# Kernel optimization log

Hardware: AMD Instinct MI355X
Metric: run time of the kernel (lower is better)

Reference implementation:

```python
import jax, jax.numpy as jnp
from jax import lax
import numpy as np

DIM = 768        # d_model (mamba-130m)
D_IN = 1024      # vision encoder feature dim
NQ = 384         # num_queries
NB = 12          # num_blocks
BATCH = 2
LSEQ = 1024      # image tokens
DI = 2 * DIM     # mamba d_inner (expand=2)
DS = 16          # d_state
DC = 4           # d_conv
DTR = 48         # dt_rank = ceil(768/16)
NH = 16          # attention heads
HD = DIM // NH
NM = NB + 2      # mamba instances: fwd-enc, bwd-enc, one per block


def _ln(x, g, b):
    m = jnp.mean(x, -1, keepdims=True)
    v = jnp.mean((x - m) ** 2, -1, keepdims=True)
    return (x - m) * lax.rsqrt(v + 1e-5) * g + b


def _mamba(x, in_w, conv_w, conv_b, xproj_w, dt_w, dt_b, A_log, Dp, out_w):
    # x: (B, L, DIM)
    Bb = x.shape[0]
    xz = x @ in_w.T                      # (B, L, 2*DI)
    xi, z = jnp.split(xz, 2, -1)
    # depthwise causal conv1d over time
    xc = lax.conv_general_dilated(xi.transpose(0, 2, 1), conv_w[:, None, :], (1,),
                                  [(DC - 1, 0)], feature_group_count=DI,
                                  dimension_numbers=('NCH', 'OIH', 'NCH'))
    xc = jax.nn.silu((xc + conv_b[None, :, None]).transpose(0, 2, 1))  # (B, L, DI)
    dbl = xc @ xproj_w.T                 # (B, L, DTR + 2*DS)
    dt, Bm, Cm = jnp.split(dbl, [DTR, DTR + DS], -1)
    dt = jax.nn.softplus(dt @ dt_w.T + dt_b)   # (B, L, DI)
    A = -jnp.exp(A_log)                        # (DI, DS)
    dA = jnp.exp(dt[..., None] * A)            # (B, L, DI, DS)
    dBx = dt[..., None] * Bm[:, :, None, :] * xc[..., None]

    def step(h, inp):
        dA_t, dBx_t, C_t = inp
        h = dA_t * h + dBx_t
        return h, jnp.einsum('bds,bs->bd', h, C_t)

    h0 = jnp.zeros((Bb, DI, DS), x.dtype)
    _, ys = lax.scan(step, h0, (dA.transpose(1, 0, 2, 3), dBx.transpose(1, 0, 2, 3), Cm.transpose(1, 0, 2)))
    y = ys.transpose(1, 0, 2) + Dp * xc
    y = y * jax.nn.silu(z)
    return y @ out_w.T


def _local_allowed(nq, nk):
    # matches Attention.get_local_mask: query i attends to its contiguous key block
    kpq, extra = nk // nq, nk % nq
    i = jnp.arange(nq)
    start = i * kpq + jnp.minimum(i, extra)
    end = start + kpq + (i < extra)
    k = jnp.arange(nk)
    return (k[None, :] >= start[:, None]) & (k[None, :] < end[:, None])


def _mha(q_in, kv, in_w, in_b, out_w, out_b, allowed):
    # nn.MultiheadAttention(dim, 16, batch_first=True) cross-attention
    wq, wk, wv = jnp.split(in_w, 3, 0)
    bq, bk, bv = jnp.split(in_b, 3, 0)
    Bb = q_in.shape[0]
    q = (q_in @ wq.T + bq).reshape(Bb, -1, NH, HD)
    k = (kv @ wk.T + bk).reshape(Bb, -1, NH, HD)
    v = (kv @ wv.T + bv).reshape(Bb, -1, NH, HD)
    s = jnp.einsum('bqhd,bkhd->bhqk', q, k) / np.float32(np.sqrt(HD))
    s = jnp.where(allowed[None, None], s, -jnp.inf)
    a = jax.nn.softmax(s, -1)
    o = jnp.einsum('bhqk,bkhd->bqhd', a, v).reshape(Bb, -1, DIM)
    return o @ out_w.T + out_b


def _model(img_emb, queries, vision_proj_w, vision_proj_b, ln_vision_g, ln_vision_b,
           mamba_in_w, mamba_conv_w, mamba_conv_b, mamba_xproj_w, mamba_dt_w, mamba_dt_b,
           mamba_A_log, mamba_D, mamba_out_w, seq_norm_g, seq_norm_b,
           attn_in_w, attn_in_b, attn_out_w, attn_out_b, cross_w, cross_b):
    mp = lambda i: (mamba_in_w[i], mamba_conv_w[i], mamba_conv_b[i], mamba_xproj_w[i],
                    mamba_dt_w[i], mamba_dt_b[i], mamba_A_log[i], mamba_D[i], mamba_out_w[i])
    feats = _ln(img_emb @ vision_proj_w.T + vision_proj_b, ln_vision_g, ln_vision_b)
    fwd = _mamba(feats, *mp(0))
    bwd = jnp.flip(_mamba(jnp.flip(feats, 1), *mp(1)), 1)
    c = fwd + bwd + feats
    x = jnp.broadcast_to(queries, (img_emb.shape[0], NQ, DIM))
    allowed = _local_allowed(NQ, c.shape[1])
    for l in range(NB):
        x = _ln(x, seq_norm_g[l], seq_norm_b[l])
        x = _mamba(x, *mp(l + 2)) + x
        score = _mha(x, c, attn_in_w[l], attn_in_b[l], attn_out_w[l], attn_out_b[l], allowed)
        x = jnp.concatenate([x, score], -1) @ cross_w[l].T + cross_b[l]
    return x


_model_jit = jax.jit(_model)


def setup_inputs() -> dict:
    key = jax.random.key(0)
    ks = iter(jax.random.split(key, 24))
    rn = lambda shape, s=0.02: jax.random.normal(next(ks), shape, jnp.float32) * s
    A_log = jnp.broadcast_to(jnp.log(jnp.arange(1, DS + 1, dtype=jnp.float32)), (NM, DI, DS))
    return {
        'img_emb': rn((BATCH, LSEQ, D_IN), 1.0),
        'queries': rn((1, NQ, DIM)),
        'vision_proj_w': rn((DIM, D_IN)),
        'vision_proj_b': jnp.zeros((DIM,), jnp.float32),
        'ln_vision_g': jnp.ones((DIM,), jnp.float32),
        'ln_vision_b': jnp.zeros((DIM,), jnp.float32),
        'mamba_in_w': rn((NM, 2 * DI, DIM)),
        'mamba_conv_w': rn((NM, DI, DC), 0.1),
        'mamba_conv_b': jnp.zeros((NM, DI), jnp.float32),
        'mamba_xproj_w': rn((NM, DTR + 2 * DS, DI)),
        'mamba_dt_w': rn((NM, DI, DTR), 0.1),
        'mamba_dt_b': rn((NM, DI), 0.5),
        'mamba_A_log': A_log,
        'mamba_D': jnp.ones((NM, DI), jnp.float32),
        'mamba_out_w': rn((NM, DIM, DI)),
        'seq_norm_g': jnp.ones((NB, DIM), jnp.float32),
        'seq_norm_b': jnp.zeros((NB, DIM), jnp.float32),
        'attn_in_w': rn((NB, 3 * DIM, DIM)),
        'attn_in_b': jnp.zeros((NB, 3 * DIM), jnp.float32),
        'attn_out_w': rn((NB, DIM, DIM)),
        'attn_out_b': jnp.zeros((NB, DIM), jnp.float32),
        'cross_w': rn((NB, DIM, 2 * DIM)),
        'cross_b': jnp.zeros((NB, DIM), jnp.float32),
    }


def reference(img_emb, queries, vision_proj_w, vision_proj_b, ln_vision_g, ln_vision_b,
              mamba_in_w, mamba_conv_w, mamba_conv_b, mamba_xproj_w, mamba_dt_w, mamba_dt_b,
              mamba_A_log, mamba_D, mamba_out_w, seq_norm_g, seq_norm_b,
              attn_in_w, attn_in_b, attn_out_w, attn_out_b, cross_w, cross_b):
    return _model_jit(img_emb, queries, vision_proj_w, vision_proj_b, ln_vision_g, ln_vision_b,
                      mamba_in_w, mamba_conv_w, mamba_conv_b, mamba_xproj_w, mamba_dt_w, mamba_dt_b,
                      mamba_A_log, mamba_D, mamba_out_w, seq_norm_g, seq_norm_b,
                      attn_in_w, attn_in_b, attn_out_w, attn_out_b, cross_w, cross_b)
```

## Files before the change

### kernel.cpp

```cpp
#include <hip/hip_runtime.h>
#include <hip/hip_bf16.h>

#define DIMQ 768
#define D_IN 1024
#define NQ 384
#define NBK 12
#define BATCH 2
#define LSEQ 1024
#define DI 1536
#define DS 16
#define DTR 48
#define NH 16
#define HD 48

typedef __attribute__((ext_vector_type(8))) short short8;
typedef __attribute__((ext_vector_type(4))) float f32x4;

#define GF_BIAS 1
#define GF_SOFTPLUS 2
#define EPI_BIAS 1
#define EPI_ADDT 2

#define LOG2E 1.4426950408889634f

__device__ __forceinline__ unsigned short f2bf(float f) {
    unsigned int u = __builtin_bit_cast(unsigned int, f);
    u = (u + 0x7FFFu + ((u >> 16) & 1u)) >> 16;
    return (unsigned short)u;
}
__device__ __forceinline__ float bf2f(unsigned short h) {
    unsigned int u = ((unsigned int)h) << 16;
    return __builtin_bit_cast(float, u);
}

__device__ __forceinline__ void gload_lds16(const void* g, void* l) {
    __builtin_amdgcn_global_load_lds(
        (const __attribute__((address_space(1))) void*)g,
        (__attribute__((address_space(3))) void*)l, 16, 0, 0);
}

struct WTab {
    const float* src[10];
    long long dstOff[10];
    long long ps[10];
    int cum[10];
    int rows[10], cols[10], dcols[10];
    int n;
    int total;
};

__global__ void wconv_kernel(unsigned short* __restrict__ dst, WTab T)
{
    const int i = blockIdx.x * 256 + threadIdx.x;
    if (i >= T.total) return;
    int sI = 0;
    while (i >= T.cum[sI]) ++sI;
    const int e = i - (sI ? T.cum[sI - 1] : 0);
    const int dcols = T.dcols[sI];
    const int r = e / dcols;
    const int c = e - r * dcols;
    float v = 0.f;
    if (r < T.rows[sI] && c < T.cols[sI]) v = T.src[sI][(long long)r * T.cols[sI] + c];
    const unsigned short h = f2bf(v);
    const unsigned short l = f2bf(v - bf2f(h));
    dst[T.dstOff[sI] + e] = h;
    dst[T.dstOff[sI] + T.ps[sI] + e] = l;
}

__global__ __launch_bounds__(256, 3)
void gemm_direct(const float* __restrict__ Ag, const unsigned short* __restrict__ Bhl,
                 float* __restrict__ Cg, const float* __restrict__ biasg,
                 int M, int N, int K, int lda, int ldb, int ldc,
                 long long sA, long long sB, long long sC, long long sBias,
                 long long planeB, int flags)
{
    __shared__ __align__(16) unsigned short As[2][2][64][40];
    __shared__ __align__(16) unsigned short Bs[2][2][128][32];

    const int z = blockIdx.z;
    const float* A = Ag + (size_t)z * sA;
    const unsigned short* Bhi = Bhl + (size_t)z * sB;
    const unsigned short* Blo = Bhi + planeB;
    float* C = Cg + (size_t)z * sC;

    const int mBase = blockIdx.x * 64;
    const int nBase = blockIdx.y * 128;
    const int tid = threadIdx.x, lane = tid & 63, wave = tid >> 6;
    const int lm = lane & 15, lq = lane >> 4;
    const int wn = wave * 32;
    const int arow = tid >> 2, aq = tid & 3;
    const int brow = lane >> 2;
    const int bcol = (lane & 3) * 8;

    const int ktiles = (K + 31) >> 5;

    auto issueB = [&](int t, int buf) {
#pragma unroll
        for (int cc = 0; cc < 4; ++cc) {
            const int chunk = wave * 4 + cc;
            const int pl = chunk >> 3;
            const int r16 = chunk & 7;
            const unsigned short* bp = pl ? Blo : Bhi;
            const int n = nBase + r16 * 16 + brow;
            gload_lds16(bp + (size_t)n * ldb + t * 32 + bcol, &Bs[buf][pl][r16 * 16][0]);
        }
    };
    auto loadA = [&](int t, float* v) {
        const int col = t * 32 + aq * 8;
        const float* src = A + (size_t)(mBase + arow) * lda + col;
#pragma unroll
        for (int u = 0; u < 2; ++u) {
            float4 t4 = make_float4(0.f, 0.f, 0.f, 0.f);
            if (col + u * 4 < K) t4 = *(const float4*)(src + u * 4);
            v[u*4+0]=t4.x; v[u*4+1]=t4.y; v[u*4+2]=t4.z; v[u*4+3]=t4.w;
        }
    };
    auto writeA = [&](const float* v, int buf) {
        short8 ph, plv;
#pragma unroll
        for (int j = 0; j < 8; ++j) {
            unsigned short h = f2bf(v[j]);
            ph[j] = (short)h;
            plv[j] = (short)f2bf(v[j] - bf2f(h));
        }
        *(short8*)&As[buf][0][arow][aq * 8] = ph;
        *(short8*)&As[buf][1][arow][aq * 8] = plv;
    };

    float av[8];
    issueB(0, 0);
    loadA(0, av);
    writeA(av, 0);

    f32x4 acc[4][2] = {};
    for (int t = 0; t < ktiles; ++t) {
        const int buf = t & 1;
        __syncthreads();
        const bool more = (t + 1) < ktiles;
        if (more) { issueB(t + 1, buf ^ 1); loadA(t + 1, av); }
        short8 ah[4], al[4], bh[2], bl[2];
#pragma unroll
        for (int i = 0; i < 4; ++i) {
            ah[i] = *(const short8*)&As[buf][0][16*i + lm][lq * 8];
            al[i] = *(const short8*)&As[buf][1][16*i + lm][lq * 8];
        }
#pragma unroll
        for (int j = 0; j < 2; ++j) {
            bh[j] = *(const short8*)&Bs[buf][0][wn + 16*j + lm][lq * 8];
            bl[j] = *(const short8*)&Bs[buf][1][wn + 16*j + lm][lq * 8];
        }
#pragma unroll
        for (int i = 0; i < 4; ++i)
#pragma unroll
            for (int j = 0; j < 2; ++j) {
                acc[i][j] = __builtin_amdgcn_mfma_f32_16x16x32_bf16(ah[i], bh[j], acc[i][j], 0, 0, 0);
                acc[i][j] = __builtin_amdgcn_mfma_f32_16x16x32_bf16(ah[i], bl[j], acc[i][j], 0, 0, 0);
                acc[i][j] = __builtin_amdgcn_mfma_f32_16x16x32_bf16(al[i], bh[j], acc[i][j], 0, 0, 0);
            }
        if (more) writeA(av, buf ^ 1);
    }

#pragma unroll
    for (int i = 0; i < 4; ++i)
#pragma unroll
        for (int j = 0; j < 2; ++j)
#pragma unroll
            for (int r = 0; r < 4; ++r) {
                const int m = mBase + i*16 + lq*4 + r;
                const int n = nBase + wn + j*16 + lm;
                float v = acc[i][j][r];
                if (flags & GF_BIAS)     v += biasg[(size_t)z * sBias + n];
                if (flags & GF_SOFTPLUS) v = (v > 20.f) ? v : log1pf(expf(v));
                C[(size_t)m * ldc + n] = v;
            }
}

__global__ __launch_bounds__(256, 3)
void gemm_splitk(const float* __restrict__ Ag, const unsigned short* __restrict__ Bhl,
                 float* __restrict__ Cp,
                 int M, int kLen, int S, int lda, int ldb, int ldP,
                 long long sA, long long sB, long long planeB)
{
    __shared__ __align__(16) unsigned short As[2][2][64][40];
    __shared__ __align__(16) unsigned short Bs[2][2][128][32];

    const int bz = blockIdx.z;
    const int s = bz % S, z = bz / S;
    const int kOff = s * kLen;
    const float* A = Ag + (size_t)z * sA;
    const unsigned short* Bhi = Bhl + (size_t)z * sB;
    const unsigned short* Blo = Bhi + planeB;

    const int mBase = blockIdx.x * 64;
    const int nBase = blockIdx.y * 128;
    const int tid = threadIdx.x, lane = tid & 63, wave = tid >> 6;
    const int lm = lane & 15, lq = lane >> 4;
    const int wn = wave * 32;
    const int arow = tid >> 2, aq = tid & 3;
    const int brow = lane >> 2;
    const int bcol = (lane & 3) * 8;

    const int ktiles = kLen >> 5;

    auto issueB = [&](int t, int buf) {
#pragma unroll
        for (int cc = 0; cc < 4; ++cc) {
            const int chunk = wave * 4 + cc;
            const int pl = chunk >> 3;
            const int r16 = chunk & 7;
            const unsigned short* bp = pl ? Blo : Bhi;
            const int n = nBase + r16 * 16 + brow;
            gload_lds16(bp + (size_t)n * ldb + kOff + t * 32 + bcol, &Bs[buf][pl][r16 * 16][0]);
        }
    };
    auto loadA = [&](int t, float* v) {
        const float* src = A + (size_t)(mBase + arow) * lda + kOff + t * 32 + aq * 8;
#pragma unroll
        for (int u = 0; u < 2; ++u) {
            const float4 t4 = *(const float4*)(src + u * 4);
            v[u*4+0]=t4.x; v[u*4+1]=t4.y; v[u*4+2]=t4.z; v[u*4+3]=t4.w;
        }
    };
    auto writeA = [&](const float* v, int buf) {
        short8 ph, plv;
#pragma unroll
        for (int j = 0; j < 8; ++j) {
            unsigned short h = f2bf(v[j]);
            ph[j] = (short)h;
            plv[j] = (short)f2bf(v[j] - bf2f(h));
        }
        *(short8*)&As[buf][0][arow][aq * 8] = ph;
        *(short8*)&As[buf][1][arow][aq * 8] = plv;
    };

    float av[8];
    issueB(0, 0);
    loadA(0, av);
    writeA(av, 0);

    f32x4 acc[4][2] = {};
    for (int t = 0; t < ktiles; ++t) {
        const int buf = t & 1;
        __syncthreads();
        const bool more = (t + 1) < ktiles;
        if (more) { issueB(t + 1, buf ^ 1); loadA(t + 1, av); }
        short8 ah[4], al[4], bh[2], bl[2];
#pragma unroll
        for (int i = 0; i < 4; ++i) {
            ah[i] = *(const short8*)&As[buf][0][16*i + lm][lq * 8];
            al[i] = *(const short8*)&As[buf][1][16*i + lm][lq * 8];
        }
#pragma unroll
        for (int j = 0; j < 2; ++j) {
            bh[j] = *(const short8*)&Bs[buf][0][wn + 16*j + lm][lq * 8];
            bl[j] = *(const short8*)&Bs[buf][1][wn + 16*j + lm][lq * 8];
        }
#pragma unroll
        for (int i = 0; i < 4; ++i)
#pragma unroll
            for (int j = 0; j < 2; ++j) {
                acc[i][j] = __builtin_amdgcn_mfma_f32_16x16x32_bf16(ah[i], bh[j], acc[i][j], 0, 0, 0);
                acc[i][j] = __builtin_amdgcn_mfma_f32_16x16x32_bf16(ah[i], bl[j], acc[i][j], 0, 0, 0);
                acc[i][j] = __builtin_amdgcn_mfma_f32_16x16x32_bf16(al[i], bh[j], acc[i][j], 0, 0, 0);
            }
        if (more) writeA(av, buf ^ 1);
    }

    float* Cb = Cp + (size_t)bz * M * ldP;
#pragma unroll
    for (int i = 0; i < 4; ++i)
#pragma unroll
        for (int j = 0; j < 2; ++j)
#pragma unroll
            for (int r = 0; r < 4; ++r) {
                const int m = mBase + i*16 + lq*4 + r;
                const int n = nBase + wn + j*16 + lm;
                Cb[(size_t)m * ldP + n] = acc[i][j][r];
            }
}

__global__ void epi_kernel(const float* __restrict__ Cp, float* __restrict__ outF,
                           const float* __restrict__ bias, const float* __restrict__ addT,
                           int Z, int S, int M, int N, int ldP, int ldOut,
                           long long sOutZ, long long sBiasZ, int ldAdd, int flags)
{
    const int n4 = N >> 2;
    const int idx = blockIdx.x * 256 + threadIdx.x;
    if (idx >= Z * M * n4) return;
    const int c4 = idx % n4;
    const int rem = idx / n4;
    const int m = rem % M;
    const int z = rem / M;
    const int n = c4 * 4;
    const float* base = Cp + ((size_t)z * S * M + m) * ldP + n;
    float4 v = *(const float4*)base;
    for (int s = 1; s < S; ++s) {
        const float4 u = *(const float4*)(base + (size_t)s * M * ldP);
        v.x += u.x; v.y += u.y; v.z += u.z; v.w += u.w;
    }
    if (flags & EPI_BIAS) {
        const float4 b4 = *(const float4*)(bias + (size_t)z * sBiasZ + n);
        v.x += b4.x; v.y += b4.y; v.z += b4.z; v.w += b4.w;
    }
    if (flags & EPI_ADDT) {
        const float4 a4 = *(const float4*)(addT + (size_t)m * ldAdd + n);
        v.x += a4.x; v.y += a4.y; v.z += a4.z; v.w += a4.w;
    }
    *(float4*)(outF + (size_t)z * sOutZ + (size_t)m * ldOut + n) = v;
}

__global__ void ln_kernel(const float* __restrict__ in, float* __restrict__ out,
                          const float* __restrict__ g, const float* __restrict__ b, int rows)
{
    const int row = blockIdx.x * 4 + (threadIdx.x >> 6);
    const int lane = threadIdx.x & 63;
    if (row >= rows) return;
    const float* p = in + (size_t)row * DIMQ;
    float v[12], s = 0.f, s2 = 0.f;
#pragma unroll
    for (int j = 0; j < 12; ++j) {
        v[j] = p[j*64 + lane];
        s += v[j];
        s2 += v[j]*v[j];
    }
#pragma unroll
    for (int o = 32; o; o >>= 1) { s += __shfl_xor(s, o); s2 += __shfl_xor(s2, o); }
    const float mean = s * (1.f/768.f);
    const float var  = s2 * (1.f/768.f) - mean*mean;
    const float inv  = rsqrtf(var + 1e-5f);
    float* q = out + (size_t)row * DIMQ;
#pragma unroll
    for (int j = 0; j < 12; ++j) {
        const int c = j*64 + lane;
        q[c] = (v[j] - mean) * inv * g[c] + b[c];
    }
}

__global__ void conv_kernel(const float* __restrict__ xz, float* __restrict__ xc,
                            const float* __restrict__ cw, const float* __restrict__ cb,
                            int Bn, int L, int instShift)
{
    const int idx = blockIdx.x * 256 + threadIdx.x;
    const int total = Bn * L * (DI/4);
    if (idx >= total) return;
    const int d4 = idx % (DI/4);
    const int t  = (idx / (DI/4)) % L;
    const int b  = idx / (L * (DI/4));
    const int inst = b >> instShift;
    const int d = d4 * 4;
    const float* base = xz + (size_t)(b * L) * 3072 + d;
    const float4 w0 = *(const float4*)(cw + (size_t)(inst*DI + d + 0) * 4);
    const float4 w1 = *(const float4*)(cw + (size_t)(inst*DI + d + 1) * 4);
    const float4 w2 = *(const float4*)(cw + (size_t)(inst*DI + d + 2) * 4);
    const float4 w3 = *(const float4*)(cw + (size_t)(inst*DI + d + 3) * 4);
    float4 acc = *(const float4*)(cb + (size_t)inst*DI + d);
    float4 xv[4];
#pragma unroll
    for (int j = 0; j < 4; ++j) {
        const int tt = t - 3 + j;
        xv[j] = (tt >= 0) ? *(const float4*)(base + (size_t)tt * 3072) : make_float4(0,0,0,0);
    }
    acc.x += xv[0].x*w0.x + xv[1].x*w0.y + xv[2].x*w0.z + xv[3].x*w0.w;
    acc.y += xv[0].y*w1.x + xv[1].y*w1.y + xv[2].y*w1.z + xv[3].y*w1.w;
    acc.z += xv[0].z*w2.x + xv[1].z*w2.y + xv[2].z*w2.z + xv[3].z*w2.w;
    acc.w += xv[0].w*w3.x + xv[1].w*w3.y + xv[2].w*w3.z + xv[3].w*w3.w;
    float4 o;
    o.x = acc.x / (1.f + expf(-acc.x));
    o.y = acc.y / (1.f + expf(-acc.y));
    o.z = acc.z / (1.f + expf(-acc.z));
    o.w = acc.w / (1.f + expf(-acc.w));
    *(float4*)(xc + (size_t)(b * L + t) * DI + d) = o;
}

__global__ __launch_bounds__(256)
void scan_p1(const float* __restrict__ dt, const float* __restrict__ dbl,
             const float* __restrict__ xc, const float* __restrict__ A_log,
             float* __restrict__ hend, float* __restrict__ sumdt,
             int L, int CL, int Bn, int instShift)
{
    const int d = blockIdx.x * 256 + threadIdx.x;
    const int b = blockIdx.y;
    const int c = blockIdx.z;
    const int inst = b >> instShift;
    const float* ap = A_log + ((size_t)inst * DI + d) * DS;
    float A2[16];
#pragma unroll
    for (int s = 0; s < 16; ++s) A2[s] = -expf(ap[s]) * LOG2E;
    float h[16] = {};
    float sd = 0.f;
    const int t0 = c * CL;
    const size_t rowbase = (size_t)b * L;
    for (int t = t0; t < t0 + CL; ++t) {
        const size_t row = rowbase + t;
        const float dtv = dt[row * DI + d];
        const float xcv = xc[row * DI + d];
        float Bv[16];
        *(float4*)(Bv + 0)  = *(const float4*)(dbl + row * 80 + 48);
        *(float4*)(Bv + 4)  = *(const float4*)(dbl + row * 80 + 52);
        *(float4*)(Bv + 8)  = *(const float4*)(dbl + row * 80 + 56);
        *(float4*)(Bv + 12) = *(const float4*)(dbl + row * 80 + 60);
        sd += dtv;
        const float bx = dtv * xcv;
#pragma unroll
        for (int s = 0; s < 16; ++s)
            h[s] = exp2f(dtv * A2[s]) * h[s] + bx * Bv[s];
    }
    float* hp = hend + (((size_t)c * Bn + b) * DI + d) * DS;
#pragma unroll
    for (int s = 0; s < 16; s += 4)
        *(float4*)(hp + s) = make_float4(h[s], h[s+1], h[s+2], h[s+3]);
    sumdt[((size_t)c * Bn + b) * DI + d] = sd;
}

__global__ void scan_p2(const float* __restrict__ hend, const float* __restrict__ sumdt,
                        const float* __restrict__ A_log, float* __restrict__ hstart,
                        int NC, int Bn, int instShift)
{
    const int gid = blockIdx.x * 256 + threadIdx.x;
    const int s = gid & 15;
    const int rem = gid >> 4;
    const int d = rem % DI;
    const int b = rem / DI;
    const int inst = b >> instShift;
    const float A2 = -expf(A_log[((size_t)inst * DI + d) * DS + s]) * LOG2E;
    float carry = 0.f;
    for (int c = 0; c < NC; ++c) {
        const size_t off = (((size_t)c * Bn + b) * DI + d) * DS + s;
        hstart[off] = carry;
        carry = exp2f(A2 * sumdt[((size_t)c * Bn + b) * DI + d]) * carry + hend[off];
    }
}

__global__ __launch_bounds__(256)
void scan_p3(const float* __restrict__ dt, const float* __restrict__ dbl,
             const float* __restrict__ xc, const float* __restrict__ xz,
             const float* __restrict__ A_log, const float* __restrict__ Dp,
             const float* __restrict__ hstart, float* __restrict__ y,
             int L, int CL, int Bn, int instShift)
{
    const int d = blockIdx.x * 256 + threadIdx.x;
    const int b = blockIdx.y;
    const int c = blockIdx.z;
    const int inst = b >> instShift;
    const float* ap = A_log + ((size_t)inst * DI + d) * DS;
    float A2[16];
#pragma unroll
    for (int s = 0; s < 16; ++s) A2[s] = -expf(ap[s]) * LOG2E;
    const float Dd = Dp[(size_t)inst * DI + d];
    float h[16];
    const float* hp = hstart + (((size_t)c * Bn + b) * DI + d) * DS;
#pragma unroll
    for (int s = 0; s < 16; s += 4) {
        const float4 t4 = *(const float4*)(hp + s);
        h[s] = t4.x; h[s+1] = t4.y; h[s+2] = t4.z; h[s+3] = t4.w;
    }
    const int t0 = c * CL;
    const size_t rowbase = (size_t)b * L;
    for (int t = t0; t < t0 + CL; ++t) {
        const size_t row = rowbase + t;
        const float dtv = dt[row * DI + d];
        const float xcv = xc[row * DI + d];
        const float zv  = xz[row * 3072 + DI + d];
        float Bv[16], Cv[16];
        *(float4*)(Bv + 0)  = *(const float4*)(dbl + row * 80 + 48);
        *(float4*)(Bv + 4)  = *(const float4*)(dbl + row * 80 + 52);
        *(float4*)(Bv + 8)  = *(const float4*)(dbl + row * 80 + 56);
        *(float4*)(Bv + 12) = *(const float4*)(dbl + row * 80 + 60);
        *(float4*)(Cv + 0)  = *(const float4*)(dbl + row * 80 + 64);
        *(float4*)(Cv + 4)  = *(const float4*)(dbl + row * 80 + 68);
        *(float4*)(Cv + 8)  = *(const float4*)(dbl + row * 80 + 72);
        *(float4*)(Cv + 12) = *(const float4*)(dbl + row * 80 + 76);
        const float bx = dtv * xcv;
#pragma unroll
        for (int s = 0; s < 16; ++s)
            h[s] = exp2f(dtv * A2[s]) * h[s] + bx * Bv[s];
        float p0 = 0.f, p1 = 0.f, p2 = 0.f, p3 = 0.f;
#pragma unroll
        for (int s = 0; s < 4; ++s) {
            p0 += h[s]      * Cv[s];
            p1 += h[s + 4]  * Cv[s + 4];
            p2 += h[s + 8]  * Cv[s + 8];
            p3 += h[s + 12] * Cv[s + 12];
        }
        const float p = (p0 + p1) + (p2 + p3);
        y[row * DI + d] = (p + Dd * xcv) * (zv / (1.f + expf(-zv)));
    }
}

__global__ void attn_kernel(const float* __restrict__ q, const float* __restrict__ kv,
                            float* __restrict__ o)
{
    const int bi = blockIdx.x;
    const int b = bi / NQ, i = bi % NQ;
    const int tid = threadIdx.x;
    const int h = tid >> 2, r = tid & 3;
    int start, len;
    if (i < 256) { start = 3*i; len = 3; } else { start = 2*i + 256; len = 2; }
    const float* qp = q + (size_t)bi * DIMQ + h*48 + r*12;
    float qv[12];
#pragma unroll
    for (int u = 0; u < 12; ++u) qv[u] = qp[u];
    float s[3] = {-1e30f, -1e30f, -1e30f};
    for (int j = 0; j < len; ++j) {
        const float* kp = kv + (size_t)(b*LSEQ + start + j) * 1536 + h*48 + r*12;
        float p = 0.f;
#pragma unroll
        for (int u = 0; u < 12; ++u) p += qv[u] * kp[u];
        p += __shfl_xor(p, 1);
        p += __shfl_xor(p, 2);
        s[j] = p * 0.14433756729740644f;
    }
    const float mx = fmaxf(s[0], fmaxf(s[1], s[2]));
    float e[3];
    e[0] = expf(s[0]-mx); e[1] = expf(s[1]-mx); e[2] = expf(s[2]-mx);
    const float inv = 1.f / (e[0] + e[1] + e[2]);
    float ov[12] = {};
    for (int j = 0; j < len; ++j) {
        const float w = e[j] * inv;
        const float* vp = kv + (size_t)(b*LSEQ + start + j) * 1536 + 768 + h*48 + r*12;
#pragma unroll
        for (int u = 0; u < 12; ++u) ov[u] += w * vp[u];
    }
    float* op = o + (size_t)bi * DIMQ + h*48 + r*12;
#pragma unroll
    for (int u = 0; u < 12; ++u) op[u] = ov[u];
}

__global__ void flip_kernel(float* __restrict__ X2)
{
    const int idx = blockIdx.x * 256 + threadIdx.x;
    if (idx >= 2*1024*192) return;
    const int d4 = idx % 192;
    const int t  = (idx / 192) % 1024;
    const int b  = idx / (192 * 1024);
    const size_t dst = ((size_t)((2+b)*1024 + t)) * DIMQ + d4*4;
    const size_t src = ((size_t)(b*1024 + (1023 - t))) * DIMQ + d4*4;
    *(float4*)(X2 + dst) = *(const float4*)(X2 + src);
}

__global__ void combine_kernel(const float* __restrict__ oe, const float* __restrict__ feats,
                               float* __restrict__ c)
{
    const int idx = blockIdx.x * 256 + threadIdx.x;
    if (idx >= 2*1024*192) return;
    const int d4 = idx % 192;
    const int t  = (idx / 192) % 1024;
    const int b  = idx / (192 * 1024);
    const size_t fw = ((size_t)(b*1024 + t)) * DIMQ + d4*4;
    const size_t bw = ((size_t)((2+b)*1024 + (1023 - t))) * DIMQ + d4*4;
    const float4 a = *(const float4*)(oe + fw);
    const float4 bb = *(const float4*)(oe + bw);
    const float4 f = *(const float4*)(feats + fw);
    float4 o;
    o.x = a.x + bb.x + f.x; o.y = a.y + bb.y + f.y;
    o.z = a.z + bb.z + f.z; o.w = a.w + bb.w + f.w;
    *(float4*)(c + fw) = o;
}

__global__ void qinit_kernel(float* __restrict__ x, const float* __restrict__ queries)
{
    const int idx = blockIdx.x * 256 + threadIdx.x;
    if (idx >= 2*NQ*192) return;
    const int d4 = idx % 192;
    const int i  = (idx / 192) % NQ;
    *(float4*)(x + (size_t)idx * 4) = *(const float4*)(queries + ((size_t)i * DIMQ + d4*4));
}

extern "C" void kernel_launch(void* const* d_in, const int* in_sizes, int n_in,
                              void* d_out, int out_size, void* d_ws, size_t ws_size,
                              hipStream_t stream) {
    const float* img_emb  = (const float*)d_in[0];
    const float* queries  = (const float*)d_in[1];
    const float* vis_w    = (const float*)d_in[2];
    const float* vis_b    = (const float*)d_in[3];
    const float* lnv_g    = (const float*)d_in[4];
    const float* lnv_b    = (const float*)d_in[5];
    const float* m_in_w   = (const float*)d_in[6];
    const float* m_conv_w = (const float*)d_in[7];
    const float* m_conv_b = (const float*)d_in[8];
    const float* m_xp_w   = (const float*)d_in[9];
    const float* m_dt_w   = (const float*)d_in[10];
    const float* m_dt_b   = (const float*)d_in[11];
    const float* m_A_log  = (const float*)d_in[12];
    const float* m_D      = (const float*)d_in[13];
    const float* m_out_w  = (const float*)d_in[14];
    const float* sn_g     = (const float*)d_in[15];
    const float* sn_b     = (const float*)d_in[16];
    const float* a_in_w   = (const float*)d_in[17];
    const float* a_in_b   = (const float*)d_in[18];
    const float* a_out_w  = (const float*)d_in[19];
    const float* a_out_b  = (const float*)d_in[20];
    const float* cr_w     = (const float*)d_in[21];
    const float* cr_b     = (const float*)d_in[22];
    float* out = (float*)d_out;

    float* ws = (float*)d_ws;
    float* X2   = ws; ws += (size_t)4096*768;
    float* xzb  = ws; ws += (size_t)4096*3072;
    float* xcb  = ws; ws += (size_t)4096*1536;
    float* dblb = ws; ws += (size_t)4096*80;
    float* dtb  = ws; ws += (size_t)4096*1536;
    float* yb   = ws; ws += (size_t)4096*1536;
    float* oe   = ws; ws += (size_t)4096*768;
    float* cbuf = ws; ws += (size_t)2048*768;
    float* xbuf = ws; ws += (size_t)768*768;
    float* xn   = ws; ws += (size_t)768*768;
    float* x1s  = ws; ws += (size_t)768*1536;
    float* qb   = ws; ws += (size_t)768*768;
    float* ob   = ws; ws += (size_t)768*768;
    float* Cp   = ws; ws += (size_t)2359296;
    unsigned short* wenc = (unsigned short*)ws; ws += (size_t)16908288/2;
    unsigned short* wlay = (unsigned short*)ws; ws += (size_t)14745600/2;

    const long long P_VIS = 768LL*1024;
    const long long P_IN  = 3072LL*768;
    const long long P_XP  = 128LL*1536;
    const long long P_DT  = 1536LL*64;
    const long long P_OUT = 768LL*1536;
    const long long P_AIN = 2304LL*768;
    const long long P_AOUT= 768LL*768;
    const long long P_CR  = 768LL*1536;
    const long long off_vis   = 0;
    const long long off_encIn = 2*P_VIS;
    const long long off_encXp = off_encIn + 4*P_IN;
    const long long off_encDt = off_encXp + 4*P_XP;
    const long long off_encOut= off_encDt + 4*P_DT;
    const long long off_in  = 0;
    const long long off_xp  = 2*P_IN;
    const long long off_dt  = off_xp + 2*P_XP;
    const long long off_out = off_dt + 2*P_DT;
    const long long off_aIn = off_out + 2*P_OUT;
    const long long off_aOut= off_aIn + 2*P_AIN;
    const long long off_cr  = off_aOut + 2*P_AOUT;

    auto addSeg = [](WTab& T, const float* src, int rows, int cols, int drows, int dcols,
                     long long dstOff) {
        const int k = T.n;
        T.src[k] = src; T.rows[k] = rows; T.cols[k] = cols; T.dcols[k] = dcols;
        T.ps[k] = (long long)drows * dcols;
        T.dstOff[k] = dstOff;
        T.total += drows * dcols;
        T.cum[k] = T.total;
        T.n = k + 1;
    };

    auto GD = [&](const float* A, const unsigned short* Bhl, long long planeB,
                  float* C, const float* bias,
                  int M, int N, int K, int lda, int ldb, int ldc,
                  long long sA, long long sB, long long sC, long long sBias,
                  int Z, int flags) {
        dim3 grid(M/64, N/128, Z);
        gemm_direct<<<grid, 256, 0, stream>>>(A, Bhl, C, bias, M, N, K, lda, ldb, ldc,
                                              sA, sB, sC, sBias, planeB, flags);
    };
    auto GS = [&](const float* A, const unsigned short* Bhl, long long planeB,
                  int M, int Ntile, int kLen, int S, int lda, int ldb, int ldP,
                  long long sA, long long sB, int Z) {
        dim3 grid(M/64, Ntile/128, Z*S);
        gemm_splitk<<<grid, 256, 0, stream>>>(A, Bhl, Cp, M, kLen, S, lda, ldb, ldP,
                                              sA, sB, planeB);
    };
    auto EPI = [&](float* outF, const float* bias, const float* addT,
                   int Z, int S, int M, int N, int ldP, int ldOut,
                   long long sOutZ, long long sBiasZ, int ldAdd, int flags) {
        const int total = Z * M * (N/4);
        epi_kernel<<<(total+255)/256, 256, 0, stream>>>(Cp, outF, bias, addT, Z, S, M, N,
                                                        ldP, ldOut, sOutZ, sBiasZ, ldAdd, flags);
    };

    {
        WTab T = {}; T.n = 0; T.total = 0;
        addSeg(T, vis_w, 768, 1024, 768, 1024, off_vis);
        addSeg(T, m_in_w,               3072, 768, 3072, 768, off_encIn);
        addSeg(T, m_in_w + 3072*768,    3072, 768, 3072, 768, off_encIn + 2*P_IN);
        addSeg(T, m_xp_w,               80, 1536, 128, 1536, off_encXp);
        addSeg(T, m_xp_w + 80*1536,     80, 1536, 128, 1536, off_encXp + 2*P_XP);
        addSeg(T, m_dt_w,               1536, 48, 1536, 64, off_encDt);
        addSeg(T, m_dt_w + 1536*48,     1536, 48, 1536, 64, off_encDt + 2*P_DT);
        addSeg(T, m_out_w,              768, 1536, 768, 1536, off_encOut);
        addSeg(T, m_out_w + 768*1536,   768, 1536, 768, 1536, off_encOut + 2*P_OUT);
        wconv_kernel<<<(T.total+255)/256, 256, 0, stream>>>(wenc, T);
    }

    GD(img_emb, wenc + off_vis, P_VIS, oe, vis_b,
       2048, 768, 1024, 1024, 1024, 768, 0,0,0,0, 1, GF_BIAS);
    ln_kernel<<<512, 256, 0, stream>>>(oe, X2, lnv_g, lnv_b, 2048);
    flip_kernel<<<(2*1024*192 + 255)/256, 256, 0, stream>>>(X2);
    qinit_kernel<<<(2*NQ*192 + 255)/256, 256, 0, stream>>>(xbuf, queries);

    GD(X2, wenc + off_encIn, P_IN, xzb, nullptr,
       2048, 3072, 768, 768, 768, 3072, 2048LL*768, 2*P_IN, 2048LL*3072, 0, 2, 0);
    conv_kernel<<<(4*1024*384 + 255)/256, 256, 0, stream>>>(xzb, xcb, m_conv_w, m_conv_b, 4, 1024, 1);
    GS(xcb, wenc + off_encXp, P_XP, 2048, 128, 384, 4, 1536, 1536, 128,
       2048LL*1536, 2*P_XP, 2);
    EPI(dblb, nullptr, nullptr, 2, 4, 2048, 80, 128, 80, 2048LL*80, 0, 0, 0);
    GD(dblb, wenc + off_encDt, P_DT, dtb, m_dt_b,
       2048, 1536, 48, 80, 64, 1536, 2048LL*80, 2*P_DT, 2048LL*1536, 1536, 2,
       GF_BIAS | GF_SOFTPLUS);
    {
        const int NC = 8, CL = 128;
        float* hend   = oe;
        float* hstart = oe + (size_t)NC*4*DI*DS;
        float* sumdt  = oe + (size_t)2*NC*4*DI*DS;
        scan_p1<<<dim3(6, 4, NC), 256, 0, stream>>>(dtb, dblb, xcb, m_A_log, hend, sumdt, 1024, CL, 4, 1);
        scan_p2<<<(4*DI*DS)/256, 256, 0, stream>>>(hend, sumdt, m_A_log, hstart, NC, 4, 1);
        scan_p3<<<dim3(6, 4, NC), 256, 0, stream>>>(dtb, dblb, xcb, xzb, m_A_log, m_D, hstart, yb, 1024, CL, 4, 1);
    }
    GD(yb, wenc + off_encOut, P_OUT, oe, nullptr,
       2048, 768, 1536, 1536, 1536, 768, 2048LL*1536, 2*P_OUT, 2048LL*768, 0, 2, 0);
    combine_kernel<<<(2*1024*192 + 255)/256, 256, 0, stream>>>(oe, X2, cbuf);

    for (int l = 0; l < NBK; ++l) {
        const int li = l + 2;
        {
            WTab T = {}; T.n = 0; T.total = 0;
            addSeg(T, m_in_w + (size_t)li*3072*768, 3072, 768, 3072, 768, off_in);
            addSeg(T, m_xp_w + (size_t)li*80*1536,  80, 1536, 128, 1536, off_xp);
            addSeg(T, m_dt_w + (size_t)li*1536*48,  1536, 48, 1536, 64, off_dt);
            addSeg(T, m_out_w + (size_t)li*768*1536, 768, 1536, 768, 1536, off_out);
            addSeg(T, a_in_w + (size_t)l*2304*768,  2304, 768, 2304, 768, off_aIn);
            addSeg(T, a_out_w + (size_t)l*768*768,  768, 768, 768, 768, off_aOut);
            addSeg(T, cr_w + (size_t)l*768*1536,    768, 1536, 768, 1536, off_cr);
            wconv_kernel<<<(T.total+255)/256, 256, 0, stream>>>(wlay, T);
        }
        ln_kernel<<<192, 256, 0, stream>>>(xbuf, xn, sn_g + (size_t)l*768, sn_b + (size_t)l*768, 768);
        GD(xn, wlay + off_in, P_IN, xzb, nullptr,
           768, 3072, 768, 768, 768, 3072, 0,0,0,0, 1, 0);
        conv_kernel<<<(2*NQ*384 + 255)/256, 256, 0, stream>>>(
            xzb, xcb, m_conv_w + (size_t)li*DI*4, m_conv_b + (size_t)li*DI, 2, NQ, 8);
        GS(xcb, wlay + off_xp, P_XP, 768, 128, 96, 16, 1536, 1536, 128, 0, 0, 1);
        EPI(dblb, nullptr, nullptr, 1, 16, 768, 80, 128, 80, 0, 0, 0, 0);
        GD(dblb, wlay + off_dt, P_DT, dtb, m_dt_b + (size_t)li*1536,
           768, 1536, 48, 80, 64, 1536, 0,0,0,0, 1, GF_BIAS | GF_SOFTPLUS);
        {
            const int NC = 12, CL = 32;
            const float* Ap = m_A_log + (size_t)li*DI*DS;
            float* hend   = oe;
            float* hstart = oe + (size_t)NC*2*DI*DS;
            float* sumdt  = oe + (size_t)2*NC*2*DI*DS;
            scan_p1<<<dim3(6, 2, NC), 256, 0, stream>>>(dtb, dblb, xcb, Ap, hend, sumdt, NQ, CL, 2, 8);
            scan_p2<<<(2*DI*DS)/256, 256, 0, stream>>>(hend, sumdt, Ap, hstart, NC, 2, 8);
            scan_p3<<<dim3(6, 2, NC), 256, 0, stream>>>(dtb, dblb, xcb, xzb, Ap, m_D + (size_t)li*DI,
                                                        hstart, yb, NQ, CL, 2, 8);
        }
        GS(yb, wlay + off_out, P_OUT, 768, 768, 384, 4, 1536, 1536, 768, 0, 0, 1);
        EPI(x1s, nullptr, xn, 1, 4, 768, 768, 768, 1536, 0, 0, 768, EPI_ADDT);
        GS(x1s, wlay + off_aIn, P_AIN, 768, 768, 192, 4, 1536, 768, 768, 0, 0, 1);
        EPI(qb, a_in_b + (size_t)l*2304, nullptr, 1, 4, 768, 768, 768, 768, 0, 0, 0, EPI_BIAS);
        GD(cbuf, wlay + off_aIn + 768LL*768, P_AIN, oe, a_in_b + (size_t)l*2304 + 768,
           2048, 1536, 768, 768, 768, 1536, 0,0,0,0, 1, GF_BIAS);
        attn_kernel<<<2*NQ, 64, 0, stream>>>(qb, oe, ob);
        GS(ob, wlay + off_aOut, P_AOUT, 768, 768, 192, 4, 768, 768, 768, 0, 0, 1);
        EPI(x1s + 768, a_out_b + (size_t)l*768, nullptr, 1, 4, 768, 768, 768, 1536, 0, 0, 0, EPI_BIAS);
        float* dst = (l == NBK - 1) ? out : xbuf;
        GS(x1s, wlay + off_cr, P_CR, 768, 768, 384, 4, 1536, 1536, 768, 0, 0, 1);
        EPI(dst, cr_b + (size_t)l*768, nullptr, 1, 4, 768, 768, 768, 768, 0, 0, 0, EPI_BIAS);
    }
}
```

Baseline: 4.336 ms.

## Fuse split-K reduction into GEMM, batch weight conversion, retune splits and scan chunks

```diff
diff --git a/kernel.cpp b/kernel.cpp
--- a/kernel.cpp
+++ b/kernel.cpp
@@ -67,6 +67,33 @@
     dst[T.dstOff[sI] + T.ps[sI] + e] = l;
 }
 
+struct LTab {
+    const float* src[7];
+    long long srcStride[7], dstOff[7], ps[7];
+    int rows[7], cols[7], dcols[7], cum[7];
+};
+
+__global__ __launch_bounds__(256)
+void wconv_layers(unsigned short* __restrict__ dst, long long layerStride, int lBase, LTab T)
+{
+    const int e = blockIdx.x * 256 + threadIdx.x;
+    const int l = blockIdx.y + lBase;
+    int sI = 0;
+    while (e >= T.cum[sI]) ++sI;
+    const int eo = e - (sI ? T.cum[sI - 1] : 0);
+    const int dc = T.dcols[sI];
+    const int r = eo / dc;
+    const int c = eo - r * dc;
+    float v = 0.f;
+    if (r < T.rows[sI] && c < T.cols[sI])
+        v = T.src[sI][(long long)l * T.srcStride[sI] + (long long)r * T.cols[sI] + c];
+    const unsigned short h = f2bf(v);
+    const unsigned short lo2 = f2bf(v - bf2f(h));
+    unsigned short* d = dst + (long long)blockIdx.y * layerStride + T.dstOff[sI];
+    d[eo] = h;
+    d[T.ps[sI] + eo] = lo2;
+}
+
 __global__ __launch_bounds__(256, 3)
 void gemm_direct(const float* __restrict__ Ag, const unsigned short* __restrict__ Bhl,
                  float* __restrict__ Cg, const float* __restrict__ biasg,
@@ -176,13 +203,16 @@
 }
 
 __global__ __launch_bounds__(256, 3)
-void gemm_splitk(const float* __restrict__ Ag, const unsigned short* __restrict__ Bhl,
-                 float* __restrict__ Cp,
-                 int M, int kLen, int S, int lda, int ldb, int ldP,
-                 long long sA, long long sB, long long planeB)
+void gemm_splitkf(const float* __restrict__ Ag, const unsigned short* __restrict__ Bhl,
+                  float* __restrict__ Cp, int* __restrict__ counters,
+                  float* __restrict__ outF, const float* __restrict__ bias,
+                  const float* __restrict__ addT,
+                  int M, int Nout, int kLen, int S, int lda, int ldb, int ldc, int ldAdd,
+                  long long sA, long long sB, long long planeB, long long sOutZ, int flags)
 {
     __shared__ __align__(16) unsigned short As[2][2][64][40];
     __shared__ __align__(16) unsigned short Bs[2][2][128][32];
+    __shared__ int lastF;
 
     const int bz = blockIdx.z;
     const int s = bz % S, z = bz / S;
@@ -193,6 +223,7 @@
 
     const int mBase = blockIdx.x * 64;
     const int nBase = blockIdx.y * 128;
+    const int ldP = gridDim.y * 128;
     const int tid = threadIdx.x, lane = tid & 63, wave = tid >> 6;
     const int lm = lane & 15, lq = lane >> 4;
     const int wn = wave * 32;
@@ -277,45 +308,54 @@
                 const int n = nBase + wn + j*16 + lm;
                 Cb[(size_t)m * ldP + n] = acc[i][j][r];
             }
-}
-
-__global__ void epi_kernel(const float* __restrict__ Cp, float* __restrict__ outF,
-                           const float* __restrict__ bias, const float* __restrict__ addT,
-                           int Z, int S, int M, int N, int ldP, int ldOut,
-                           long long sOutZ, long long sBiasZ, int ldAdd, int flags)
-{
-    const int n4 = N >> 2;
-    const int idx = blockIdx.x * 256 + threadIdx.x;
-    if (idx >= Z * M * n4) return;
-    const int c4 = idx % n4;
-    const int rem = idx / n4;
-    const int m = rem % M;
-    const int z = rem / M;
-    const int n = c4 * 4;
-    const float* base = Cp + ((size_t)z * S * M + m) * ldP + n;
-    float4 v = *(const float4*)base;
-    for (int s = 1; s < S; ++s) {
-        const float4 u = *(const float4*)(base + (size_t)s * M * ldP);
-        v.x += u.x; v.y += u.y; v.z += u.z; v.w += u.w;
-    }
-    if (flags & EPI_BIAS) {
-        const float4 b4 = *(const float4*)(bias + (size_t)z * sBiasZ + n);
-        v.x += b4.x; v.y += b4.y; v.z += b4.z; v.w += b4.w;
-    }
-    if (flags & EPI_ADDT) {
-        const float4 a4 = *(const float4*)(addT + (size_t)m * ldAdd + n);
-        v.x += a4.x; v.y += a4.y; v.z += a4.z; v.w += a4.w;
-    }
-    *(float4*)(outF + (size_t)z * sOutZ + (size_t)m * ldOut + n) = v;
+
+    __syncthreads();
+    const int cidx = z * (gridDim.x * gridDim.y) + blockIdx.y * gridDim.x + blockIdx.x;
+    if (tid == 0) {
+        __threadfence();
+        const int prev = __hip_atomic_fetch_add(&counters[cidx], 1,
+                                                __ATOMIC_ACQ_REL, __HIP_MEMORY_SCOPE_AGENT);
+        lastF = (prev == S - 1);
+        if (prev == S - 1) {
+            __hip_atomic_store(&counters[cidx], 0, __ATOMIC_RELAXED, __HIP_MEMORY_SCOPE_AGENT);
+            __threadfence();
+        }
+    }
+    __syncthreads();
+    if (!lastF) return;
+
+    const float* Pz = Cp + (size_t)z * S * M * ldP;
+#pragma unroll
+    for (int rr = 0; rr < 8; ++rr) {
+        const int m = mBase + rr * 8 + (tid >> 5);
+        const int n = nBase + (tid & 31) * 4;
+        const float* pp = Pz + (size_t)m * ldP + n;
+        float4 v = *(const float4*)pp;
+        for (int q = 1; q < S; ++q) {
+            const float4 u = *(const float4*)(pp + (size_t)q * M * ldP);
+            v.x += u.x; v.y += u.y; v.z += u.z; v.w += u.w;
+        }
+        if (flags & EPI_BIAS) {
+            const float4 b4 = *(const float4*)(bias + n);
+            v.x += b4.x; v.y += b4.y; v.z += b4.z; v.w += b4.w;
+        }
+        if (flags & EPI_ADDT) {
+            const float4 a4 = *(const float4*)(addT + (size_t)m * ldAdd + n);
+            v.x += a4.x; v.y += a4.y; v.z += a4.z; v.w += a4.w;
+        }
+        if (n < Nout)
+            *(float4*)(outF + (size_t)z * sOutZ + (size_t)m * ldc + n) = v;
+    }
 }
 
 __global__ void ln_kernel(const float* __restrict__ in, float* __restrict__ out,
-                          const float* __restrict__ g, const float* __restrict__ b, int rows)
+                          const float* __restrict__ g, const float* __restrict__ b,
+                          int rows, int srcMod)
 {
     const int row = blockIdx.x * 4 + (threadIdx.x >> 6);
     const int lane = threadIdx.x & 63;
     if (row >= rows) return;
-    const float* p = in + (size_t)row * DIMQ;
+    const float* p = in + (size_t)(row % srcMod) * DIMQ;
     float v[12], s = 0.f, s2 = 0.f;
 #pragma unroll
     for (int j = 0; j < 12; ++j) {
@@ -555,15 +595,6 @@
     o.x = a.x + bb.x + f.x; o.y = a.y + bb.y + f.y;
     o.z = a.z + bb.z + f.z; o.w = a.w + bb.w + f.w;
     *(float4*)(c + fw) = o;
-}
-
-__global__ void qinit_kernel(float* __restrict__ x, const float* __restrict__ queries)
-{
-    const int idx = blockIdx.x * 256 + threadIdx.x;
-    if (idx >= 2*NQ*192) return;
-    const int d4 = idx % 192;
-    const int i  = (idx / 192) % NQ;
-    *(float4*)(x + (size_t)idx * 4) = *(const float4*)(queries + ((size_t)i * DIMQ + d4*4));
 }
 
 extern "C" void kernel_launch(void* const* d_in, const int* in_sizes, int n_in,
@@ -595,22 +626,30 @@
     float* out = (float*)d_out;
 
     float* ws = (float*)d_ws;
-    float* X2   = ws; ws += (size_t)4096*768;
-    float* xzb  = ws; ws += (size_t)4096*3072;
-    float* xcb  = ws; ws += (size_t)4096*1536;
-    float* dblb = ws; ws += (size_t)4096*80;
-    float* dtb  = ws; ws += (size_t)4096*1536;
-    float* yb   = ws; ws += (size_t)4096*1536;
-    float* oe   = ws; ws += (size_t)4096*768;
-    float* cbuf = ws; ws += (size_t)2048*768;
-    float* xbuf = ws; ws += (size_t)768*768;
-    float* xn   = ws; ws += (size_t)768*768;
-    float* x1s  = ws; ws += (size_t)768*1536;
-    float* qb   = ws; ws += (size_t)768*768;
-    float* ob   = ws; ws += (size_t)768*768;
-    float* Cp   = ws; ws += (size_t)2359296;
-    unsigned short* wenc = (unsigned short*)ws; ws += (size_t)16908288/2;
-    unsigned short* wlay = (unsigned short*)ws; ws += (size_t)14745600/2;
+    auto alloc = [&](size_t n) { float* p = ws; ws += n; return p; };
+    float* X2   = alloc((size_t)4096*768);
+    float* xzb  = alloc((size_t)4096*3072);
+    float* xcb  = alloc((size_t)4096*1536);
+    float* dblb = alloc((size_t)4096*80);
+    float* dtb  = alloc((size_t)4096*1536);
+    float* yb   = alloc((size_t)4096*1536);
+    float* oe   = alloc((size_t)4096*768);
+    float* cbuf = alloc((size_t)2048*768);
+    float* xbuf = alloc((size_t)768*768);
+    float* xn   = alloc((size_t)768*768);
+    float* x1s  = alloc((size_t)768*1536);
+    float* qb   = alloc((size_t)768*768);
+    float* ob   = alloc((size_t)768*768);
+    int*   cnt  = (int*)alloc(512);
+    unsigned short* wenc = (unsigned short*)alloc((size_t)16908288/2);
+
+    float* Cp = dtb;
+
+    const long long LAYER_USH = 14745600;
+    const size_t usedFloats = (size_t)(ws - (float*)d_ws);
+    const size_t needFull = (usedFloats + (size_t)12 * (LAYER_USH/2)) * 4;
+    const bool bigW = ws_size >= needFull;
+    unsigned short* wlayAll = (unsigned short*)ws;
 
     const long long P_VIS = 768LL*1024;
     const long long P_IN  = 3072LL*768;
@@ -653,20 +692,16 @@
         gemm_direct<<<grid, 256, 0, stream>>>(A, Bhl, C, bias, M, N, K, lda, ldb, ldc,
                                               sA, sB, sC, sBias, planeB, flags);
     };
-    auto GS = [&](const float* A, const unsigned short* Bhl, long long planeB,
-                  int M, int Ntile, int kLen, int S, int lda, int ldb, int ldP,
-                  long long sA, long long sB, int Z) {
-        dim3 grid(M/64, Ntile/128, Z*S);
-        gemm_splitk<<<grid, 256, 0, stream>>>(A, Bhl, Cp, M, kLen, S, lda, ldb, ldP,
-                                              sA, sB, planeB);
+    auto GSF = [&](const float* A, const unsigned short* Bhl, long long planeB,
+                   float* outF, const float* bias, const float* addT,
+                   int M, int N, int Nout, int K, int S, int lda, int ldb, int ldc, int ldAdd,
+                   long long sA, long long sB, long long sOutZ, int Z, int flags) {
+        dim3 grid(M/64, N/128, Z*S);
+        gemm_splitkf<<<grid, 256, 0, stream>>>(A, Bhl, Cp, cnt, outF, bias, addT,
+            M, Nout, K/S, S, lda, ldb, ldc, ldAdd, sA, sB, planeB, sOutZ, flags);
     };
-    auto EPI = [&](float* outF, const float* bias, const float* addT,
-                   int Z, int S, int M, int N, int ldP, int ldOut,
-                   long long sOutZ, long long sBiasZ, int ldAdd, int flags) {
-        const int total = Z * M * (N/4);
-        epi_kernel<<<(total+255)/256, 256, 0, stream>>>(Cp, outF, bias, addT, Z, S, M, N,
-                                                        ldP, ldOut, sOutZ, sBiasZ, ldAdd, flags);
-    };
+
+    hipMemsetAsync(cnt, 0, 2048, stream);
 
     {
         WTab T = {}; T.n = 0; T.total = 0;
@@ -682,26 +717,44 @@
         wconv_kernel<<<(T.total+255)/256, 256, 0, stream>>>(wenc, T);
     }
 
-    GD(img_emb, wenc + off_vis, P_VIS, oe, vis_b,
-       2048, 768, 1024, 1024, 1024, 768, 0,0,0,0, 1, GF_BIAS);
-    ln_kernel<<<512, 256, 0, stream>>>(oe, X2, lnv_g, lnv_b, 2048);
+    LTab LT = {};
+    {
+        auto seg = [&](int k, const float* src, long long srcStride, int rows, int cols,
+                       int drows, int dcols, long long dstOff) {
+            LT.src[k] = src; LT.srcStride[k] = srcStride;
+            LT.rows[k] = rows; LT.cols[k] = cols; LT.dcols[k] = dcols;
+            LT.ps[k] = (long long)drows * dcols; LT.dstOff[k] = dstOff;
+            LT.cum[k] = (k ? LT.cum[k-1] : 0) + drows * dcols;
+        };
+        seg(0, m_in_w  + (size_t)2*3072*768, 3072LL*768, 3072, 768, 3072, 768, off_in);
+        seg(1, m_xp_w  + (size_t)2*80*1536,  80LL*1536,  80, 1536, 128, 1536, off_xp);
+        seg(2, m_dt_w  + (size_t)2*1536*48,  1536LL*48,  1536, 48, 1536, 64, off_dt);
+        seg(3, m_out_w + (size_t)2*768*1536, 768LL*1536, 768, 1536, 768, 1536, off_out);
+        seg(4, a_in_w,  2304LL*768, 2304, 768, 2304, 768, off_aIn);
+        seg(5, a_out_w, 768LL*768,  768, 768, 768, 768, off_aOut);
+        seg(6, cr_w,    768LL*1536, 768, 1536, 768, 1536, off_cr);
+    }
+    if (bigW)
+        wconv_layers<<<dim3(28800, 12), 256, 0, stream>>>(wlayAll, LAYER_USH, 0, LT);
+
+    GSF(img_emb, wenc + off_vis, P_VIS, oe, vis_b, nullptr,
+        2048, 768, 768, 1024, 4, 1024, 1024, 768, 0, 0, 0, 0, 1, EPI_BIAS);
+    ln_kernel<<<512, 256, 0, stream>>>(oe, X2, lnv_g, lnv_b, 2048, 2048);
     flip_kernel<<<(2*1024*192 + 255)/256, 256, 0, stream>>>(X2);
-    qinit_kernel<<<(2*NQ*192 + 255)/256, 256, 0, stream>>>(xbuf, queries);
 
     GD(X2, wenc + off_encIn, P_IN, xzb, nullptr,
        2048, 3072, 768, 768, 768, 3072, 2048LL*768, 2*P_IN, 2048LL*3072, 0, 2, 0);
     conv_kernel<<<(4*1024*384 + 255)/256, 256, 0, stream>>>(xzb, xcb, m_conv_w, m_conv_b, 4, 1024, 1);
-    GS(xcb, wenc + off_encXp, P_XP, 2048, 128, 384, 4, 1536, 1536, 128,
-       2048LL*1536, 2*P_XP, 2);
-    EPI(dblb, nullptr, nullptr, 2, 4, 2048, 80, 128, 80, 2048LL*80, 0, 0, 0);
+    GSF(xcb, wenc + off_encXp, P_XP, dblb, nullptr, nullptr,
+        2048, 128, 80, 1536, 8, 1536, 1536, 80, 0, 2048LL*1536, 2*P_XP, 2048LL*80, 2, 0);
     GD(dblb, wenc + off_encDt, P_DT, dtb, m_dt_b,
        2048, 1536, 48, 80, 64, 1536, 2048LL*80, 2*P_DT, 2048LL*1536, 1536, 2,
        GF_BIAS | GF_SOFTPLUS);
     {
-        const int NC = 8, CL = 128;
+        const int NC = 16, CL = 64;
         float* hend   = oe;
         float* hstart = oe + (size_t)NC*4*DI*DS;
-        float* sumdt  = oe + (size_t)2*NC*4*DI*DS;
+        float* sumdt  = cbuf;
         scan_p1<<<dim3(6, 4, NC), 256, 0, stream>>>(dtb, dblb, xcb, m_A_log, hend, sumdt, 1024, CL, 4, 1);
         scan_p2<<<(4*DI*DS)/256, 256, 0, stream>>>(hend, sumdt, m_A_log, hstart, NC, 4, 1);
         scan_p3<<<dim3(6, 4, NC), 256, 0, stream>>>(dtb, dblb, xcb, xzb, m_A_log, m_D, hstart, yb, 1024, CL, 4, 1);
@@ -712,28 +765,23 @@
 
     for (int l = 0; l < NBK; ++l) {
         const int li = l + 2;
-        {
-            WTab T = {}; T.n = 0; T.total = 0;
-            addSeg(T, m_in_w + (size_t)li*3072*768, 3072, 768, 3072, 768, off_in);
-            addSeg(T, m_xp_w + (size_t)li*80*1536,  80, 1536, 128, 1536, off_xp);
-            addSeg(T, m_dt_w + (size_t)li*1536*48,  1536, 48, 1536, 64, off_dt);
-            addSeg(T, m_out_w + (size_t)li*768*1536, 768, 1536, 768, 1536, off_out);
-            addSeg(T, a_in_w + (size_t)l*2304*768,  2304, 768, 2304, 768, off_aIn);
-            addSeg(T, a_out_w + (size_t)l*768*768,  768, 768, 768, 768, off_aOut);
-            addSeg(T, cr_w + (size_t)l*768*1536,    768, 1536, 768, 1536, off_cr);
-            wconv_kernel<<<(T.total+255)/256, 256, 0, stream>>>(wlay, T);
-        }
-        ln_kernel<<<192, 256, 0, stream>>>(xbuf, xn, sn_g + (size_t)l*768, sn_b + (size_t)l*768, 768);
-        GD(xn, wlay + off_in, P_IN, xzb, nullptr,
+        const unsigned short* wl = bigW ? wlayAll + (size_t)l * LAYER_USH : wlayAll;
+        if (!bigW)
+            wconv_layers<<<dim3(28800, 1), 256, 0, stream>>>((unsigned short*)wlayAll, LAYER_USH, l, LT);
+
+        ln_kernel<<<192, 256, 0, stream>>>(l == 0 ? queries : xbuf, xn,
+                                           sn_g + (size_t)l*768, sn_b + (size_t)l*768,
+                                           768, l == 0 ? 384 : 768);
+        GD(xn, wl + off_in, P_IN, xzb, nullptr,
            768, 3072, 768, 768, 768, 3072, 0,0,0,0, 1, 0);
         conv_kernel<<<(2*NQ*384 + 255)/256, 256, 0, stream>>>(
             xzb, xcb, m_conv_w + (size_t)li*DI*4, m_conv_b + (size_t)li*DI, 2, NQ, 8);
-        GS(xcb, wlay + off_xp, P_XP, 768, 128, 96, 16, 1536, 1536, 128, 0, 0, 1);
-        EPI(dblb, nullptr, nullptr, 1, 16, 768, 80, 128, 80, 0, 0, 0, 0);
-        GD(dblb, wlay + off_dt, P_DT, dtb, m_dt_b + (size_t)li*1536,
+        GSF(xcb, wl + off_xp, P_XP, dblb, nullptr, nullptr,
+            768, 128, 80, 1536, 24, 1536, 1536, 80, 0, 0, 0, 0, 1, 0);
+        GD(dblb, wl + off_dt, P_DT, dtb, m_dt_b + (size_t)li*1536,
            768, 1536, 48, 80, 64, 1536, 0,0,0,0, 1, GF_BIAS | GF_SOFTPLUS);
         {
-            const int NC = 12, CL = 32;
+            const int NC = 24, CL = 16;
             const float* Ap = m_A_log + (size_t)li*DI*DS;
             float* hend   = oe;
             float* hstart = oe + (size_t)NC*2*DI*DS;
@@ -743,17 +791,17 @@
             scan_p3<<<dim3(6, 2, NC), 256, 0, stream>>>(dtb, dblb, xcb, xzb, Ap, m_D + (size_t)li*DI,
                                                         hstart, yb, NQ, CL, 2, 8);
         }
-        GS(yb, wlay + off_out, P_OUT, 768, 768, 384, 4, 1536, 1536, 768, 0, 0, 1);
-        EPI(x1s, nullptr, xn, 1, 4, 768, 768, 768, 1536, 0, 0, 768, EPI_ADDT);
-        GS(x1s, wlay + off_aIn, P_AIN, 768, 768, 192, 4, 1536, 768, 768, 0, 0, 1);
-        EPI(qb, a_in_b + (size_t)l*2304, nullptr, 1, 4, 768, 768, 768, 768, 0, 0, 0, EPI_BIAS);
-        GD(cbuf, wlay + off_aIn + 768LL*768, P_AIN, oe, a_in_b + (size_t)l*2304 + 768,
+        GSF(yb, wl + off_out, P_OUT, x1s, nullptr, xn,
+            768, 768, 768, 1536, 8, 1536, 1536, 1536, 768, 0, 0, 0, 1, EPI_ADDT);
+        GSF(x1s, wl + off_aIn, P_AIN, qb, a_in_b + (size_t)l*2304, nullptr,
+            768, 768, 768, 768, 8, 1536, 768, 768, 0, 0, 0, 0, 1, EPI_BIAS);
+        GD(cbuf, wl + off_aIn + 768LL*768, P_AIN, oe, a_in_b + (size_t)l*2304 + 768,
            2048, 1536, 768, 768, 768, 1536, 0,0,0,0, 1, GF_BIAS);
         attn_kernel<<<2*NQ, 64, 0, stream>>>(qb, oe, ob);
-        GS(ob, wlay + off_aOut, P_AOUT, 768, 768, 192, 4, 768, 768, 768, 0, 0, 1);
-        EPI(x1s + 768, a_out_b + (size_t)l*768, nullptr, 1, 4, 768, 768, 768, 1536, 0, 0, 0, EPI_BIAS);
+        GSF(ob, wl + off_aOut, P_AOUT, x1s + 768, a_out_b + (size_t)l*768, nullptr,
+            768, 768, 768, 768, 8, 768, 768, 1536, 0, 0, 0, 0, 1, EPI_BIAS);
         float* dst = (l == NBK - 1) ? out : xbuf;
-        GS(x1s, wlay + off_cr, P_CR, 768, 768, 384, 4, 1536, 1536, 768, 0, 0, 1);
-        EPI(dst, cr_b + (size_t)l*768, nullptr, 1, 4, 768, 768, 768, 768, 0, 0, 0, EPI_BIAS);
-    }
-}
+        GSF(x1s, wl + off_cr, P_CR, dst, cr_b + (size_t)l*768, nullptr,
+            768, 768, 768, 1536, 8, 1536, 1536, 768, 0, 0, 0, 0, 1, EPI_BIAS);
+    }
+}
```

Result: slower. 7.501 ms (+73.0%).
